# Performance work log

Measured on AMD Instinct MI355X. Metric: run time of the kernel, lower is better.

Reference implementation:

```python
import jax, jax.numpy as jnp
import numpy as np

C1, C2 = 128, 128

def _glorot(key, shape):
    fan_in = shape[-1]
    return jax.random.normal(key, shape, dtype=jnp.float32) / np.sqrt(fan_in)

def setup_inputs() -> dict:
    key = jax.random.key(0)
    ks = jax.random.split(key, 12)
    b, n = 16, 64
    x = jax.random.normal(ks[0], (b, n, 16), dtype=jnp.float32)
    # 1x1 Conv1d weights stored as [out, in]
    e1_w = _glorot(ks[1], (128, 3));    e1_b = jnp.zeros((128,), jnp.float32)
    e2_w = _glorot(ks[2], (128, 13));   e2_b = jnp.zeros((128,), jnp.float32)
    r1_w = _glorot(ks[3], (256, 128));  r1_b = jnp.zeros((256,), jnp.float32)
    r2_w = _glorot(ks[4], (512, 256));  r2_b = jnp.zeros((512,), jnp.float32)
    r3_w = _glorot(ks[5], (1024, 512)); r3_b = jnp.zeros((1024,), jnp.float32)
    w1   = _glorot(ks[6], (512, 2048)); b1   = jnp.zeros((512,), jnp.float32)
    w2   = _glorot(ks[7], (2048, 512)); b2   = jnp.zeros((2048,), jnp.float32)
    return {"x": x, "e1_w": e1_w, "e1_b": e1_b, "e2_w": e2_w, "e2_b": e2_b,
            "r1_w": r1_w, "r1_b": r1_b, "r2_w": r2_w, "r2_b": r2_b,
            "r3_w": r3_w, "r3_b": r3_b, "w1": w1, "b1": b1, "w2": w2, "b2": b2}

def reference(x, e1_w, e1_b, e2_w, e2_b, r1_w, r1_b, r2_w, r2_b, r3_w, r3_b, w1, b1, w2, b2):
    # x: [b, n, 16]; coord = first 3 dims, pos = last 13 (one-hot-like keypoint id)
    coord, pos = x[:, :, :3], x[:, :, 3:]
    # 1x1 Conv1d == per-point linear. E1/E2 each have their own ReLU, then sum.
    emb = (jax.nn.relu(jnp.einsum('bnc,oc->bno', coord, e1_w) + e1_b)
           + jax.nn.relu(jnp.einsum('bnc,oc->bno', pos, e2_w) + e2_b))  # [b,n,128]
    # refine_E: three 1x1 conv + relu stages -> [b,n,1024]
    emb = jax.nn.relu(jnp.einsum('bnc,oc->bno', emb, r1_w) + r1_b)
    emb = jax.nn.relu(jnp.einsum('bnc,oc->bno', emb, r2_w) + r2_b)
    emb = jax.nn.relu(jnp.einsum('bnc,oc->bno', emb, r3_w) + r3_b)
    # Pairwise layer1: cat((emb_i, emb_j), ch) with emb_i[b,c,i,j]=emb[b,c,j],
    # emb_j[b,c,i,j]=emb[b,c,i]. A 1x1 conv on the concat decomposes into
    # two matmuls applied to emb, broadcast-added pairwise (never forming the
    # [b,2048,n,n] tensor).
    w1a, w1b = w1[:, :1024], w1[:, 1024:]
    A = jnp.einsum('bnc,oc->bno', emb, w1a)  # depends on j
    B = jnp.einsum('bnc,oc->bno', emb, w1b)  # depends on i
    h1 = jax.nn.relu(B[:, :, None, :] + A[:, None, :, :] + b1)  # [b,i,j,512]
    # reduction='mean' over (i,j); layer2 (1x1 conv, linear) commutes with mean
    m = jnp.mean(h1, axis=(1, 2))                 # [b,512]
    out = jnp.einsum('bc,oc->bo', m, w2) + b2     # [b,2048]
    return out
```

## Files before the change

### kernel.cpp

```cpp
#include <hip/hip_runtime.h>


typedef __attribute__((ext_vector_type(8))) short s16x8;
typedef __attribute__((ext_vector_type(8))) unsigned short u16x8;
typedef __attribute__((ext_vector_type(4))) float f32x4;

#define NBLK 512
#define MAGIC 0xA5C3961Du

static __device__ __forceinline__ unsigned short f2bf(float f) {
    unsigned u = __float_as_uint(f);
    u += 0x7fff + ((u >> 16) & 1);
    return (unsigned short)(u >> 16);
}

static __device__ __forceinline__ unsigned cvtpk(float lo, float hi) {
    unsigned r;
    asm("v_cvt_pk_bf16_f32 %0, %1, %2" : "=v"(r) : "v"(lo), "v"(hi));
    return r;
}

static __device__ __forceinline__ unsigned agl_u32(const unsigned* p) {
    return __hip_atomic_load(p, __ATOMIC_RELAXED, __HIP_MEMORY_SCOPE_AGENT);
}
static __device__ __forceinline__ void ags_u32(unsigned* p, unsigned v) {
    __hip_atomic_store(p, v, __ATOMIC_RELAXED, __HIP_MEMORY_SCOPE_AGENT);
}
static __device__ __forceinline__ void ags_f32(float* p, float v) {
    __hip_atomic_store(p, v, __ATOMIC_RELAXED, __HIP_MEMORY_SCOPE_AGENT);
}
static __device__ __forceinline__ void ags_u16(unsigned short* p, unsigned short v) {
    __hip_atomic_store(p, v, __ATOMIC_RELAXED, __HIP_MEMORY_SCOPE_AGENT);
}

static __device__ __forceinline__ void flag_set(unsigned* f) {
    __syncthreads();
    if (threadIdx.x == 0) ags_u32(f, MAGIC);
}
static __device__ __forceinline__ void wait_range(const unsigned* f, int n) {
    if ((int)threadIdx.x < n)
        while (agl_u32(&f[threadIdx.x]) != MAGIC) __builtin_amdgcn_s_sleep(1);
    __syncthreads();
}

static __device__ void gemm_stage(
    char* smem, int K, int tn, int wgather,
    const unsigned short* __restrict__ A,
    const float* __restrict__ Wf,
    const float* __restrict__ bias, int relu,
    unsigned short* __restrict__ Cb, float* __restrict__ Cf, int N,
    const unsigned* __restrict__ fdep, int ndep,
    unsigned* __restrict__ fout)
{
    unsigned short* As = (unsigned short*)smem;
    unsigned short* Ws = (unsigned short*)(smem + 32 * 72 * 2);
    int t = threadIdx.x;
    int tile = blockIdx.x;
    int m0 = (tile / tn) * 32, n0 = (tile % tn) * 64;
    int lane = t & 63, wv = t >> 6;
    int wm = (wv >> 1) * 16, wn = (wv & 1) * 32;
    int lr = lane & 15, quad = lane >> 4;
    int srow = t >> 3, scol = (t & 7) * 8;

    int r0 = n0 + srow, r1 = n0 + srow + 32;
    const float* w0p = wgather ? Wf + (size_t)(r0 & 511) * 2048 + ((size_t)(r0 >> 9) << 10)
                               : Wf + (size_t)r0 * K;
    const float* w1p = wgather ? Wf + (size_t)(r1 & 511) * 2048 + ((size_t)(r1 >> 9) << 10)
                               : Wf + (size_t)r1 * K;

    float4 wa0 = *(const float4*)(w0p + scol), wa1 = *(const float4*)(w0p + scol + 4);
    float4 wb0 = *(const float4*)(w1p + scol), wb1 = *(const float4*)(w1p + scol + 4);

    wait_range(fdep, ndep);

    const unsigned short* Ap = A + (size_t)(m0 + srow) * K + scol;
    u16x8 ra = *(const u16x8*)Ap;

    f32x4 acc[2] = {};
    for (int k0 = 0; k0 < K; k0 += 64) {
        __syncthreads();
        {
            union { unsigned u[4]; u16x8 v; } pw0, pw1;
            pw0.u[0] = cvtpk(wa0.x, wa0.y); pw0.u[1] = cvtpk(wa0.z, wa0.w);
            pw0.u[2] = cvtpk(wa1.x, wa1.y); pw0.u[3] = cvtpk(wa1.z, wa1.w);
            pw1.u[0] = cvtpk(wb0.x, wb0.y); pw1.u[1] = cvtpk(wb0.z, wb0.w);
            pw1.u[2] = cvtpk(wb1.x, wb1.y); pw1.u[3] = cvtpk(wb1.z, wb1.w);
            *(u16x8*)(As + srow * 72 + scol)        = ra;
            *(u16x8*)(Ws + srow * 72 + scol)        = pw0.v;
            *(u16x8*)(Ws + (srow + 32) * 72 + scol) = pw1.v;
        }
        __syncthreads();
        if (k0 + 64 < K) {
            ra = *(const u16x8*)(Ap + k0 + 64);
            int fo = k0 + 64 + scol;
            wa0 = *(const float4*)(w0p + fo); wa1 = *(const float4*)(w0p + fo + 4);
            wb0 = *(const float4*)(w1p + fo); wb1 = *(const float4*)(w1p + fo + 4);
        }
#pragma unroll
        for (int kk = 0; kk < 64; kk += 32) {
            s16x8 af  = *(const s16x8*)(As + (wm + lr) * 72 + kk + quad * 8);
            s16x8 bf0 = *(const s16x8*)(Ws + (wn + lr) * 72 + kk + quad * 8);
            s16x8 bf1 = *(const s16x8*)(Ws + (wn + 16 + lr) * 72 + kk + quad * 8);
            acc[0] = __builtin_amdgcn_mfma_f32_16x16x32_bf16(af, bf0, acc[0], 0, 0, 0);
            acc[1] = __builtin_amdgcn_mfma_f32_16x16x32_bf16(af, bf1, acc[1], 0, 0, 0);
        }
    }

#pragma unroll
    for (int nt = 0; nt < 2; ++nt) {
        int col = n0 + wn + nt * 16 + lr;
        float bv = bias ? bias[col] : 0.f;
#pragma unroll
        for (int r = 0; r < 4; ++r) {
            int row = m0 + wm + quad * 4 + r;
            float v = acc[nt][r] + bv;
            if (relu) v = fmaxf(v, 0.f);
            if (Cb) ags_u16(Cb + (size_t)row * N + col, f2bf(v));
            else    ags_f32(Cf + (size_t)row * N + col, v);
        }
    }
    flag_set(fout);
}

static __device__ void stage1(
    char* smem,
    const float* __restrict__ x,
    const float* __restrict__ e1w, const float* __restrict__ e1b,
    const float* __restrict__ e2w, const float* __restrict__ e2b,
    const float* __restrict__ r1w, const float* __restrict__ r1b,
    unsigned short* __restrict__ emb1b, unsigned* __restrict__ f1)
{
    unsigned short* As = (unsigned short*)smem;
    unsigned short* Ws = (unsigned short*)(smem + 32 * 136 * 2);
    int t = threadIdx.x;
    int i = blockIdx.x;
    int m0 = (i >> 2) * 32, n0 = (i & 3) * 64;

    {
        int row = t >> 3, c0 = (t & 7) * 16;
        const float* xr = x + (size_t)(m0 + row) * 16;
        float4 xv0 = *(const float4*)(xr);
        float4 xv1 = *(const float4*)(xr + 4);
        float4 xv2 = *(const float4*)(xr + 8);
        float4 xv3 = *(const float4*)(xr + 12);
        float xv[16] = {xv0.x, xv0.y, xv0.z, xv0.w, xv1.x, xv1.y, xv1.z, xv1.w,
                        xv2.x, xv2.y, xv2.z, xv2.w, xv3.x, xv3.y, xv3.z, xv3.w};
        union { unsigned u[4]; u16x8 v; } pk0, pk1;
#pragma unroll
        for (int e = 0; e < 16; e += 2) {
            float o2[2];
#pragma unroll
            for (int h = 0; h < 2; ++h) {
                int o = c0 + e + h;
                float s1 = e1b[o] + xv[0] * e1w[o * 3] + xv[1] * e1w[o * 3 + 1]
                                  + xv[2] * e1w[o * 3 + 2];
                float s2 = e2b[o];
#pragma unroll
                for (int k = 0; k < 13; ++k) s2 += xv[3 + k] * e2w[o * 13 + k];
                o2[h] = fmaxf(s1, 0.f) + fmaxf(s2, 0.f);
            }
            unsigned pv = cvtpk(o2[0], o2[1]);
            if (e < 8) pk0.u[e >> 1] = pv; else pk1.u[(e - 8) >> 1] = pv;
        }
        *(u16x8*)(As + row * 136 + c0)     = pk0.v;
        *(u16x8*)(As + row * 136 + c0 + 8) = pk1.v;
    }

    int lane = t & 63, wv = t >> 6;
    int wm = (wv >> 1) * 16, wn = (wv & 1) * 32;
    int lr = lane & 15, quad = lane >> 4;
    int srow = t >> 3, scol = (t & 7) * 8;
    const float* w0p = r1w + (size_t)(n0 + srow) * 128;
    const float* w1p = r1w + (size_t)(n0 + srow + 32) * 128;
    float4 wa0 = *(const float4*)(w0p + scol), wa1 = *(const float4*)(w0p + scol + 4);
    float4 wb0 = *(const float4*)(w1p + scol), wb1 = *(const float4*)(w1p + scol + 4);

    f32x4 acc[2] = {};
    __syncthreads();
    for (int k0 = 0; k0 < 128; k0 += 64) {
        if (k0) __syncthreads();
        {
            union { unsigned u[4]; u16x8 v; } pw0, pw1;
            pw0.u[0] = cvtpk(wa0.x, wa0.y); pw0.u[1] = cvtpk(wa0.z, wa0.w);
            pw0.u[2] = cvtpk(wa1.x, wa1.y); pw0.u[3] = cvtpk(wa1.z, wa1.w);
            pw1.u[0] = cvtpk(wb0.x, wb0.y); pw1.u[1] = cvtpk(wb0.z, wb0.w);
            pw1.u[2] = cvtpk(wb1.x, wb1.y); pw1.u[3] = cvtpk(wb1.z, wb1.w);
            *(u16x8*)(Ws + srow * 72 + scol)        = pw0.v;
            *(u16x8*)(Ws + (srow + 32) * 72 + scol) = pw1.v;
        }
        __syncthreads();
        if (k0 + 64 < 128) {
            int fo = k0 + 64 + scol;
            wa0 = *(const float4*)(w0p + fo); wa1 = *(const float4*)(w0p + fo + 4);
            wb0 = *(const float4*)(w1p + fo); wb1 = *(const float4*)(w1p + fo + 4);
        }
#pragma unroll
        for (int kk = 0; kk < 64; kk += 32) {
            s16x8 af  = *(const s16x8*)(As + (wm + lr) * 136 + k0 + kk + quad * 8);
            s16x8 bf0 = *(const s16x8*)(Ws + (wn + lr) * 72 + kk + quad * 8);
            s16x8 bf1 = *(const s16x8*)(Ws + (wn + 16 + lr) * 72 + kk + quad * 8);
            acc[0] = __builtin_amdgcn_mfma_f32_16x16x32_bf16(af, bf0, acc[0], 0, 0, 0);
            acc[1] = __builtin_amdgcn_mfma_f32_16x16x32_bf16(af, bf1, acc[1], 0, 0, 0);
        }
    }

#pragma unroll
    for (int nt = 0; nt < 2; ++nt) {
        int col = n0 + wn + nt * 16 + lr;
        float bv = r1b[col];
#pragma unroll
        for (int r = 0; r < 4; ++r) {
            int row = m0 + wm + quad * 4 + r;
            ags_u16(emb1b + (size_t)row * 256 + col, f2bf(fmaxf(acc[nt][r] + bv, 0.f)));
        }
    }
    flag_set(&f1[i]);
}

static __device__ void stage5(
    char* smem,
    const float* __restrict__ AB, const float* __restrict__ b1,
    float* __restrict__ pmsum,
    const unsigned* __restrict__ f4, unsigned* __restrict__ f5)
{
    float* sA  = (float*)smem;
    float* sB  = (float*)(smem + 16384);
    float* sb1 = (float*)(smem + 20480);
    float (*sPart)[64] = (float(*)[64])(smem + 20736);
    int u = blockIdx.x;
    int t = threadIdx.x;
    int b = u & 15, cb = (u >> 4) & 7, z = u >> 7;
    int c0 = cb * 64;
    int cl = t & 63, ig = t >> 6;

    if (t < 4) {
        int m = 2 * b + (t & 1), nn = cb + (t >> 1) * 8;
        while (agl_u32(&f4[m * 16 + nn]) != MAGIC) __builtin_amdgcn_s_sleep(1);
    }
    __syncthreads();

#pragma unroll
    for (int rep = 0; rep < 4; ++rep) {
        int lin = rep * 256 + t;
        int j = lin >> 4, cq = (lin & 15) * 4;
        float4 v = *(const float4*)(AB + (size_t)(b * 64 + j) * 1024 + c0 + cq);
        *(float4*)&sA[j * 64 + cq] = v;
    }
    {
        int i2 = t >> 4, cq = (t & 15) * 4;
        float4 v = *(const float4*)(AB + (size_t)(b * 64 + z * 16 + i2) * 1024 + 512 + c0 + cq);
        *(float4*)&sB[i2 * 64 + cq] = v;
    }
    if (t < 64) sb1[t] = b1[c0 + t];
    __syncthreads();

    float av[64];
#pragma unroll
    for (int j = 0; j < 64; ++j) av[j] = sA[j * 64 + cl];
    float b1c = sb1[cl];
    float s = 0.f;
#pragma unroll
    for (int ii = 0; ii < 4; ++ii) {
        float base = sB[(ig * 4 + ii) * 64 + cl] + b1c;
#pragma unroll
        for (int j = 0; j < 64; ++j) s += fmaxf(base + av[j], 0.f);
    }
    sPart[ig][cl] = s;
    __syncthreads();
    if (t < 64) {
        float tot = sPart[0][t] + sPart[1][t] + sPart[2][t] + sPart[3][t];
        ags_f32(&pmsum[((size_t)(b * 4 + z) * 8 + cb) * 64 + t], tot);
    }
    if (t == 0) {
        asm volatile("s_waitcnt vmcnt(0)" ::: "memory");
        ags_u32(&f5[u], MAGIC);
    }
}

static __device__ void stage6(
    char* smem,
    const float* __restrict__ pmsum, const float* __restrict__ w2,
    const float* __restrict__ b2, float* __restrict__ out,
    const unsigned* __restrict__ f5)
{
    float* sm = (float*)smem;
    int u = blockIdx.x;
    int t = threadIdx.x;
    int b = u & 15, ob = u >> 4;
    if (t < 32)
        while (agl_u32(&f5[b + 16 * t]) != MAGIC) __builtin_amdgcn_s_sleep(1);
    __syncthreads();
#pragma unroll
    for (int h = 0; h < 2; ++h) {
        int c = h * 256 + t;
        int cb = c >> 6, cl = c & 63;
        float s = 0.f;
#pragma unroll
        for (int z = 0; z < 4; ++z)
            s += pmsum[((size_t)(b * 4 + z) * 8 + cb) * 64 + cl];
        sm[c] = s * (1.f / 4096.f);
    }
    __syncthreads();
    int o = ob * 256 + t;
    const float* wr = w2 + (size_t)o * 512;
    float acc = 0.f;
#pragma unroll 8
    for (int c = 0; c < 512; c += 4) {
        float4 w = *(const float4*)(wr + c);
        acc += sm[c] * w.x + sm[c + 1] * w.y + sm[c + 2] * w.z + sm[c + 3] * w.w;
    }
    out[b * 2048 + o] = acc + b2[o];
}

__global__ __launch_bounds__(256, 2) void k_mega(
    const float* __restrict__ x,
    const float* __restrict__ e1w, const float* __restrict__ e1b,
    const float* __restrict__ e2w, const float* __restrict__ e2b,
    const float* __restrict__ r1w, const float* __restrict__ r1b,
    const float* __restrict__ r2w, const float* __restrict__ r2b,
    const float* __restrict__ r3w, const float* __restrict__ r3b,
    const float* __restrict__ w1,  const float* __restrict__ b1,
    const float* __restrict__ w2,  const float* __restrict__ b2,
    float* __restrict__ out,
    unsigned short* __restrict__ emb1b, unsigned short* __restrict__ emb2b,
    unsigned short* __restrict__ emb3b,
    float* __restrict__ AB, float* __restrict__ pmsum,
    unsigned* __restrict__ f1, unsigned* __restrict__ f2,
    unsigned* __restrict__ f3, unsigned* __restrict__ f4,
    unsigned* __restrict__ f5)
{
    __shared__ __attribute__((aligned(16))) char smem[21760];
    int i = blockIdx.x;

    if (threadIdx.x == 0)
        __builtin_amdgcn_fence(__ATOMIC_ACQUIRE, "agent");
    __syncthreads();

    if (i < 128)
        stage1(smem, x, e1w, e1b, e2w, e2b, r1w, r1b, emb1b, f1);

    if (i < 256)
        gemm_stage(smem, 256, 8, 0, emb1b, r2w, r2b, 1, emb2b, nullptr, 512,
                   &f1[(i >> 3) * 4], 4, &f2[i]);

    gemm_stage(smem, 512, 16, 0, emb2b, r3w, r3b, 1, emb3b, nullptr, 1024,
               &f2[(i >> 4) * 8], 8, &f3[i]);

    gemm_stage(smem, 1024, 16, 1, emb3b, w1, nullptr, 0, nullptr, AB, 1024,
               &f3[(i >> 4) * 16], 16, &f4[i]);

    stage5(smem, AB, b1, pmsum, f4, f5);

    if (i < 128)
        stage6(smem, pmsum, w2, b2, out, f5);
}

extern "C" void kernel_launch(void* const* d_in, const int* in_sizes, int n_in,
                              void* d_out, int out_size, void* d_ws, size_t ws_size,
                              hipStream_t stream)
{
    const float* x   = (const float*)d_in[0];
    const float* e1w = (const float*)d_in[1];
    const float* e1b = (const float*)d_in[2];
    const float* e2w = (const float*)d_in[3];
    const float* e2b = (const float*)d_in[4];
    const float* r1w = (const float*)d_in[5];
    const float* r1b = (const float*)d_in[6];
    const float* r2w = (const float*)d_in[7];
    const float* r2b = (const float*)d_in[8];
    const float* r3w = (const float*)d_in[9];
    const float* r3b = (const float*)d_in[10];
    const float* w1  = (const float*)d_in[11];
    const float* b1  = (const float*)d_in[12];
    const float* w2  = (const float*)d_in[13];
    const float* b2  = (const float*)d_in[14];
    float* out = (float*)d_out;

    unsigned short* emb1b = (unsigned short*)d_ws;
    unsigned short* emb2b = emb1b + 1024 * 256;
    unsigned short* emb3b = emb2b + 1024 * 512;
    float* AB    = (float*)(emb3b + 1024 * 1024);
    float* pmsum = AB + 1024 * 1024;
    unsigned* f1 = (unsigned*)(pmsum + 16 * 4 * 8 * 64);
    unsigned* f2 = f1 + 128;
    unsigned* f3 = f2 + 256;
    unsigned* f4 = f3 + 512;
    unsigned* f5 = f4 + 512;

    k_mega<<<NBLK, 256, 0, stream>>>(
        x, e1w, e1b, e2w, e2b, r1w, r1b, r2w, r2b, r3w, r3b,
        w1, b1, w2, b2, out,
        emb1b, emb2b, emb3b, AB, pmsum, f1, f2, f3, f4, f5);
}
```

Baseline: 144.1 us.

## Use 128-wide K chunks and wait only on the producer flags each chunk needs

The GEMM stages now stage 128-element K chunks in shared memory, using a padded row stride of 132 elements, instead of 64-wide chunks. This halves the number of barrier-separated iterations. The all-dependencies wait before the loop is replaced by a per-chunk spin on only the two producer tiles that cover that chunk's columns. This lets consumer blocks start computing before every upstream tile has finished. Stage1 loads the full r1 weight tile once and does a single MFMA pass, at the cost of more registers per thread and every thread spinning on the flags itself.

Measured after the change: 195.3 us. 35.5% more time.

```diff
diff --git a/kernel.cpp b/kernel.cpp
--- a/kernel.cpp
+++ b/kernel.cpp
@@ -7,6 +7,7 @@
 
 #define NBLK 512
 #define MAGIC 0xA5C3961Du
+#define LDA 132
 
 static __device__ __forceinline__ unsigned short f2bf(float f) {
     unsigned u = __float_as_uint(f);
@@ -37,10 +38,10 @@
     __syncthreads();
     if (threadIdx.x == 0) ags_u32(f, MAGIC);
 }
-static __device__ __forceinline__ void wait_range(const unsigned* f, int n) {
-    if ((int)threadIdx.x < n)
-        while (agl_u32(&f[threadIdx.x]) != MAGIC) __builtin_amdgcn_s_sleep(1);
-    __syncthreads();
+static __device__ __forceinline__ void wait2(const unsigned* f, int j) {
+    while (agl_u32(&f[2 * j]) != MAGIC)     __builtin_amdgcn_s_sleep(1);
+    while (agl_u32(&f[2 * j + 1]) != MAGIC) __builtin_amdgcn_s_sleep(1);
+    asm volatile("" ::: "memory");
 }
 
 static __device__ void gemm_stage(
@@ -49,58 +50,63 @@
     const float* __restrict__ Wf,
     const float* __restrict__ bias, int relu,
     unsigned short* __restrict__ Cb, float* __restrict__ Cf, int N,
-    const unsigned* __restrict__ fdep, int ndep,
-    unsigned* __restrict__ fout)
+    const unsigned* __restrict__ fdep, unsigned* __restrict__ fout)
 {
     unsigned short* As = (unsigned short*)smem;
-    unsigned short* Ws = (unsigned short*)(smem + 32 * 72 * 2);
+    unsigned short* Ws = (unsigned short*)(smem + 32 * LDA * 2);
     int t = threadIdx.x;
     int tile = blockIdx.x;
     int m0 = (tile / tn) * 32, n0 = (tile % tn) * 64;
     int lane = t & 63, wv = t >> 6;
     int wm = (wv >> 1) * 16, wn = (wv & 1) * 32;
     int lr = lane & 15, quad = lane >> 4;
-    int srow = t >> 3, scol = (t & 7) * 8;
-
-    int r0 = n0 + srow, r1 = n0 + srow + 32;
-    const float* w0p = wgather ? Wf + (size_t)(r0 & 511) * 2048 + ((size_t)(r0 >> 9) << 10)
-                               : Wf + (size_t)r0 * K;
-    const float* w1p = wgather ? Wf + (size_t)(r1 & 511) * 2048 + ((size_t)(r1 >> 9) << 10)
-                               : Wf + (size_t)r1 * K;
-
-    float4 wa0 = *(const float4*)(w0p + scol), wa1 = *(const float4*)(w0p + scol + 4);
-    float4 wb0 = *(const float4*)(w1p + scol), wb1 = *(const float4*)(w1p + scol + 4);
-
-    wait_range(fdep, ndep);
-
-    const unsigned short* Ap = A + (size_t)(m0 + srow) * K + scol;
-    u16x8 ra = *(const u16x8*)Ap;
+
+    int arow = t >> 3, acol = (t & 7) * 16;
+    int wrow = t >> 2, wcol = (t & 3) * 32;
+    int gr = n0 + wrow;
+    const float* wp = wgather ? Wf + (size_t)(gr & 511) * 2048 + ((size_t)(gr >> 9) << 10)
+                              : Wf + (size_t)gr * K;
+    const unsigned short* Ap = A + (size_t)(m0 + arow) * K + acol;
+
+    int nch = K >> 7;
+    float4 wr[8];
+    u16x8 ar0, ar1;
+
+#pragma unroll
+    for (int q = 0; q < 8; ++q) wr[q] = *(const float4*)(wp + wcol + q * 4);
+    wait2(fdep, 0);
+    ar0 = *(const u16x8*)(Ap);
+    ar1 = *(const u16x8*)(Ap + 8);
 
     f32x4 acc[2] = {};
-    for (int k0 = 0; k0 < K; k0 += 64) {
+    for (int j = 0; j < nch; ++j) {
         __syncthreads();
         {
-            union { unsigned u[4]; u16x8 v; } pw0, pw1;
-            pw0.u[0] = cvtpk(wa0.x, wa0.y); pw0.u[1] = cvtpk(wa0.z, wa0.w);
-            pw0.u[2] = cvtpk(wa1.x, wa1.y); pw0.u[3] = cvtpk(wa1.z, wa1.w);
-            pw1.u[0] = cvtpk(wb0.x, wb0.y); pw1.u[1] = cvtpk(wb0.z, wb0.w);
-            pw1.u[2] = cvtpk(wb1.x, wb1.y); pw1.u[3] = cvtpk(wb1.z, wb1.w);
-            *(u16x8*)(As + srow * 72 + scol)        = ra;
-            *(u16x8*)(Ws + srow * 72 + scol)        = pw0.v;
-            *(u16x8*)(Ws + (srow + 32) * 72 + scol) = pw1.v;
+            union { unsigned u[4]; u16x8 v; } pk;
+#pragma unroll
+            for (int s = 0; s < 4; ++s) {
+                float4 a = wr[2 * s], b = wr[2 * s + 1];
+                pk.u[0] = cvtpk(a.x, a.y); pk.u[1] = cvtpk(a.z, a.w);
+                pk.u[2] = cvtpk(b.x, b.y); pk.u[3] = cvtpk(b.z, b.w);
+                *(u16x8*)(Ws + wrow * LDA + wcol + s * 8) = pk.v;
+            }
+            *(u16x8*)(As + arow * LDA + acol)     = ar0;
+            *(u16x8*)(As + arow * LDA + acol + 8) = ar1;
         }
         __syncthreads();
-        if (k0 + 64 < K) {
-            ra = *(const u16x8*)(Ap + k0 + 64);
-            int fo = k0 + 64 + scol;
-            wa0 = *(const float4*)(w0p + fo); wa1 = *(const float4*)(w0p + fo + 4);
-            wb0 = *(const float4*)(w1p + fo); wb1 = *(const float4*)(w1p + fo + 4);
-        }
-#pragma unroll
-        for (int kk = 0; kk < 64; kk += 32) {
-            s16x8 af  = *(const s16x8*)(As + (wm + lr) * 72 + kk + quad * 8);
-            s16x8 bf0 = *(const s16x8*)(Ws + (wn + lr) * 72 + kk + quad * 8);
-            s16x8 bf1 = *(const s16x8*)(Ws + (wn + 16 + lr) * 72 + kk + quad * 8);
+        if (j + 1 < nch) {
+            int ko = (j + 1) << 7;
+#pragma unroll
+            for (int q = 0; q < 8; ++q) wr[q] = *(const float4*)(wp + ko + wcol + q * 4);
+            wait2(fdep, j + 1);
+            ar0 = *(const u16x8*)(Ap + ko);
+            ar1 = *(const u16x8*)(Ap + ko + 8);
+        }
+#pragma unroll
+        for (int kk = 0; kk < 128; kk += 32) {
+            s16x8 af  = *(const s16x8*)(As + (wm + lr) * LDA + kk + quad * 8);
+            s16x8 bf0 = *(const s16x8*)(Ws + (wn + lr) * LDA + kk + quad * 8);
+            s16x8 bf1 = *(const s16x8*)(Ws + (wn + 16 + lr) * LDA + kk + quad * 8);
             acc[0] = __builtin_amdgcn_mfma_f32_16x16x32_bf16(af, bf0, acc[0], 0, 0, 0);
             acc[1] = __builtin_amdgcn_mfma_f32_16x16x32_bf16(af, bf1, acc[1], 0, 0, 0);
         }
@@ -131,10 +137,16 @@
     unsigned short* __restrict__ emb1b, unsigned* __restrict__ f1)
 {
     unsigned short* As = (unsigned short*)smem;
-    unsigned short* Ws = (unsigned short*)(smem + 32 * 136 * 2);
+    unsigned short* Ws = (unsigned short*)(smem + 32 * LDA * 2);
     int t = threadIdx.x;
     int i = blockIdx.x;
     int m0 = (i >> 2) * 32, n0 = (i & 3) * 64;
+
+    int wrow = t >> 2, wcol = (t & 3) * 32;
+    const float* wp = r1w + (size_t)(n0 + wrow) * 128;
+    float4 wr[8];
+#pragma unroll
+    for (int q = 0; q < 8; ++q) wr[q] = *(const float4*)(wp + wcol + q * 4);
 
     {
         int row = t >> 3, c0 = (t & 7) * 16;
@@ -162,46 +174,33 @@
             unsigned pv = cvtpk(o2[0], o2[1]);
             if (e < 8) pk0.u[e >> 1] = pv; else pk1.u[(e - 8) >> 1] = pv;
         }
-        *(u16x8*)(As + row * 136 + c0)     = pk0.v;
-        *(u16x8*)(As + row * 136 + c0 + 8) = pk1.v;
-    }
+        *(u16x8*)(As + row * LDA + c0)     = pk0.v;
+        *(u16x8*)(As + row * LDA + c0 + 8) = pk1.v;
+    }
+    __syncthreads();
+    {
+        union { unsigned u[4]; u16x8 v; } pk;
+#pragma unroll
+        for (int s = 0; s < 4; ++s) {
+            float4 a = wr[2 * s], b = wr[2 * s + 1];
+            pk.u[0] = cvtpk(a.x, a.y); pk.u[1] = cvtpk(a.z, a.w);
+            pk.u[2] = cvtpk(b.x, b.y); pk.u[3] = cvtpk(b.z, b.w);
+            *(u16x8*)(Ws + wrow * LDA + wcol + s * 8) = pk.v;
+        }
+    }
+    __syncthreads();
 
     int lane = t & 63, wv = t >> 6;
     int wm = (wv >> 1) * 16, wn = (wv & 1) * 32;
     int lr = lane & 15, quad = lane >> 4;
-    int srow = t >> 3, scol = (t & 7) * 8;
-    const float* w0p = r1w + (size_t)(n0 + srow) * 128;
-    const float* w1p = r1w + (size_t)(n0 + srow + 32) * 128;
-    float4 wa0 = *(const float4*)(w0p + scol), wa1 = *(const float4*)(w0p + scol + 4);
-    float4 wb0 = *(const float4*)(w1p + scol), wb1 = *(const float4*)(w1p + scol + 4);
-
     f32x4 acc[2] = {};
-    __syncthreads();
-    for (int k0 = 0; k0 < 128; k0 += 64) {
-        if (k0) __syncthreads();
-        {
-            union { unsigned u[4]; u16x8 v; } pw0, pw1;
-            pw0.u[0] = cvtpk(wa0.x, wa0.y); pw0.u[1] = cvtpk(wa0.z, wa0.w);
-            pw0.u[2] = cvtpk(wa1.x, wa1.y); pw0.u[3] = cvtpk(wa1.z, wa1.w);
-            pw1.u[0] = cvtpk(wb0.x, wb0.y); pw1.u[1] = cvtpk(wb0.z, wb0.w);
-            pw1.u[2] = cvtpk(wb1.x, wb1.y); pw1.u[3] = cvtpk(wb1.z, wb1.w);
-            *(u16x8*)(Ws + srow * 72 + scol)        = pw0.v;
-            *(u16x8*)(Ws + (srow + 32) * 72 + scol) = pw1.v;
-        }
-        __syncthreads();
-        if (k0 + 64 < 128) {
-            int fo = k0 + 64 + scol;
-            wa0 = *(const float4*)(w0p + fo); wa1 = *(const float4*)(w0p + fo + 4);
-            wb0 = *(const float4*)(w1p + fo); wb1 = *(const float4*)(w1p + fo + 4);
-        }
-#pragma unroll
-        for (int kk = 0; kk < 64; kk += 32) {
-            s16x8 af  = *(const s16x8*)(As + (wm + lr) * 136 + k0 + kk + quad * 8);
-            s16x8 bf0 = *(const s16x8*)(Ws + (wn + lr) * 72 + kk + quad * 8);
-            s16x8 bf1 = *(const s16x8*)(Ws + (wn + 16 + lr) * 72 + kk + quad * 8);
-            acc[0] = __builtin_amdgcn_mfma_f32_16x16x32_bf16(af, bf0, acc[0], 0, 0, 0);
-            acc[1] = __builtin_amdgcn_mfma_f32_16x16x32_bf16(af, bf1, acc[1], 0, 0, 0);
-        }
+#pragma unroll
+    for (int kk = 0; kk < 128; kk += 32) {
+        s16x8 af  = *(const s16x8*)(As + (wm + lr) * LDA + kk + quad * 8);
+        s16x8 bf0 = *(const s16x8*)(Ws + (wn + lr) * LDA + kk + quad * 8);
+        s16x8 bf1 = *(const s16x8*)(Ws + (wn + 16 + lr) * LDA + kk + quad * 8);
+        acc[0] = __builtin_amdgcn_mfma_f32_16x16x32_bf16(af, bf0, acc[0], 0, 0, 0);
+        acc[1] = __builtin_amdgcn_mfma_f32_16x16x32_bf16(af, bf1, acc[1], 0, 0, 0);
     }
 
 #pragma unroll
@@ -329,7 +328,7 @@
     unsigned* __restrict__ f3, unsigned* __restrict__ f4,
     unsigned* __restrict__ f5)
 {
-    __shared__ __attribute__((aligned(16))) char smem[21760];
+    __shared__ __attribute__((aligned(16))) char smem[32 * LDA * 2 + 64 * LDA * 2];
     int i = blockIdx.x;
 
     if (threadIdx.x == 0)
@@ -341,13 +340,13 @@
 
     if (i < 256)
         gemm_stage(smem, 256, 8, 0, emb1b, r2w, r2b, 1, emb2b, nullptr, 512,
-                   &f1[(i >> 3) * 4], 4, &f2[i]);
+                   &f1[(i >> 3) * 4], &f2[i]);
 
     gemm_stage(smem, 512, 16, 0, emb2b, r3w, r3b, 1, emb3b, nullptr, 1024,
-               &f2[(i >> 4) * 8], 8, &f3[i]);
+               &f2[(i >> 4) * 8], &f3[i]);
 
     gemm_stage(smem, 1024, 16, 1, emb3b, w1, nullptr, 0, nullptr, AB, 1024,
-               &f3[(i >> 4) * 16], 16, &f4[i]);
+               &f3[(i >> 4) * 16], &f4[i]);
 
     stage5(smem, AB, b1, pmsum, f4, f5);
 
```
